# Kernel tuning notes

Hardware: AMD Instinct MI355X
Metric: run time of the kernel (lower is better)

## Reference

```python
import jax, jax.numpy as jnp
import numpy as np

USER_NUM = 100000
ITEM_NUM = 50000
N = USER_NUM + ITEM_NUM
D = 64
NNZ = 2400000
B = 4096
NLEVEL = 3
LEAF = 32
HID = 256
NCLS = 2
NLAYERS = 2
EPS = 0.1
TAU = 0.2


def _l2norm(x, axis=-1):
    return x / jnp.clip(jnp.linalg.norm(x, axis=axis, keepdims=True), 1e-12)


def setup_inputs():
    key = jax.random.key(0)
    ks = jax.random.split(key, 32)
    def w(k, shape):
        fan = shape[-2] if len(shape) >= 2 else shape[-1]
        return jax.random.normal(k, shape, jnp.float32) / np.sqrt(fan)
    z = lambda *s: jnp.zeros(s, jnp.float32)
    return {
        "ego_emb": w(ks[0], (N, D)),
        "gc_w": w(ks[1], (NLAYERS, D, D)), "gc_b": z(NLAYERS, D),
        "bi_w": w(ks[2], (NLAYERS, D, D)), "bi_b": z(NLAYERS, D),
        "uh_w": w(ks[3], (NLEVEL, D, D)), "uh_b": z(NLEVEL, D),
        "ih_w": w(ks[4], (NLEVEL, D, D)), "ih_b": z(NLEVEL, D),
        "ud_w1": w(ks[5], (NLEVEL, D, HID)), "ud_b1": z(NLEVEL, HID),
        "ud_w2": w(ks[6], (NLEVEL, HID, LEAF)), "ud_b2": z(NLEVEL, LEAF),
        "id_w1": w(ks[7], (NLEVEL, D, HID)), "id_b1": z(NLEVEL, HID),
        "id_w2": w(ks[8], (NLEVEL, HID, LEAF)), "id_b2": z(NLEVEL, LEAF),
        "q_w": w(ks[9], (LEAF, LEAF)), "q_b": z(LEAF),
        "k_w": w(ks[10], (LEAF, LEAF)), "k_b": z(LEAF),
        "v_w": w(ks[11], (LEAF, LEAF)), "v_b": z(LEAF),
        "dg_w1": w(ks[12], (NLEVEL * LEAF, D)), "dg_b1": z(D),
        "dg_w2": w(ks[13], (D, D)), "dg_b2": z(D),
        "pr_w": w(ks[14], (D, NCLS)), "pr_b": z(NCLS),
        "adj_vals": jax.random.uniform(ks[15], (NNZ,), jnp.float32) / 16.0,
        "hier_skills": jax.random.uniform(ks[16], (B, NLEVEL * LEAF), jnp.float32),
        "user_id": jax.random.randint(ks[17], (B,), 0, USER_NUM),
        "item_id": jax.random.randint(ks[18], (B,), 0, ITEM_NUM),
        "adj_rows": jax.random.randint(ks[19], (NNZ,), 0, N),
        "adj_cols": jax.random.randint(ks[20], (NNZ,), 0, N),
    }


def _sam(x, q_w, q_b, k_w, k_b, v_w, v_b):
    # x: [B, S, d], single-head self-attention (n_heads=1)
    d = x.shape[-1]
    q = x @ q_w + q_b
    k = x @ k_w + k_b
    v = x @ v_w + v_b
    scores = jnp.einsum('bsd,btd->bst', q, k) / jnp.sqrt(jnp.float32(d))
    attn = jax.nn.softmax(scores, axis=-1)  # softmax over key axis t
    return jnp.einsum('bst,btd->bsd', attn, v)


def _cl_loss(v1, v2):
    n1 = _l2norm(v1)
    n2 = _l2norm(v2)
    pos = jnp.exp(jnp.sum(n1 * n2, -1) / TAU)
    ttl = jnp.sum(jnp.exp(n1 @ n2.T / TAU), axis=1)
    return jnp.mean(-jnp.log(pos / ttl))


def _cl_module(recs, key):
    # recs: [L, B, LEAF]
    noise = jax.random.uniform(key, recs.shape, recs.dtype)
    recs_new = recs + jnp.sign(recs) * _l2norm(noise) * EPS
    return jnp.mean(jax.vmap(_cl_loss)(recs, recs_new))


def reference(ego_emb, gc_w, gc_b, bi_w, bi_b, uh_w, uh_b, ih_w, ih_b,
              ud_w1, ud_b1, ud_w2, ud_b2, id_w1, id_b1, id_w2, id_b2,
              q_w, q_b, k_w, k_b, v_w, v_b, dg_w1, dg_b1, dg_w2, dg_b2,
              pr_w, pr_b, adj_vals, hier_skills, user_id, item_id,
              adj_rows, adj_cols):
    # ---- NGCF propagation: sparse adj matmul + bi-interaction ----
    E = ego_emb
    E_sum = ego_emb
    for l in range(NLAYERS):
        side = jax.ops.segment_sum(adj_vals[:, None] * E[adj_cols], adj_rows,
                                   num_segments=N)  # spmm(adj_norm, E)
        sum_e = jax.nn.leaky_relu(side @ gc_w[l] + gc_b[l])
        bi_e = jax.nn.leaky_relu((E * side) @ bi_w[l] + bi_b[l])
        E = _l2norm(sum_e + bi_e)  # dropout -> identity (eval)
        E_sum = E_sum + E
    ue = E_sum[:USER_NUM][user_id]   # [B, D]
    ie = E_sum[USER_NUM:][item_id]   # [B, D]
    # ---- hierarchy projections + disentangled encoders (stacked over levels) ----
    u_reps = jnp.tanh(jnp.einsum('bd,lde->lbe', ue, uh_w) + uh_b[:, None, :])
    i_reps = jnp.tanh(jnp.einsum('bd,lde->lbe', ie, ih_w) + ih_b[:, None, :])
    u_recs = jnp.einsum('lbh,lhk->lbk',
                        jnp.tanh(jnp.einsum('lbd,ldh->lbh', u_reps, ud_w1) + ud_b1[:, None, :]),
                        ud_w2) + ud_b2[:, None, :]  # [L, B, LEAF]
    i_recs = jnp.einsum('lbh,lhk->lbk',
                        jnp.tanh(jnp.einsum('lbd,ldh->lbh', i_reps, id_w1) + id_b1[:, None, :]),
                        id_w2) + id_b2[:, None, :]
    # ---- self-attention across levels ----
    u_att = _sam(u_recs.transpose(1, 0, 2), q_w, q_b, k_w, k_b, v_w, v_b)  # [B, L, LEAF]
    i_att = _sam(i_recs.transpose(1, 0, 2), q_w, q_b, k_w, k_b, v_w, v_b)
    # ---- contrastive losses (detached in original via torch.Tensor(...)) ----
    kc = jax.random.split(jax.random.key(42), 2)
    cl = _cl_module(u_att.transpose(1, 0, 2), kc[0]) + _cl_module(i_att.transpose(1, 0, 2), kc[1])
    cl = jax.lax.stop_gradient(cl)
    # ---- diagnosis head ----
    skills = hier_skills.reshape(B, NLEVEL, LEAF)
    diag = ((jax.nn.sigmoid(u_att) - jax.nn.sigmoid(i_att)) * skills).reshape(B, NLEVEL * LEAF)
    h = jnp.tanh(diag @ dg_w1 + dg_b1) @ dg_w2 + dg_b2  # dropout -> identity (eval)
    out = jax.nn.softmax(h @ pr_w + pr_b, axis=-1)
    return (out, cl)
```

## Files before the change

kernel.cpp:

```cpp
#include <hip/hip_runtime.h>
#include <stdint.h>
#include <math.h>

#define USER_N 100000
#define NODE_N 150000
#define DD 64
#define NNZE 2400000
#define BB 4096
#define NLV 3
#define LF 32
#define HALF_SZ 196608u
#define NTILE 586
#define NSUB 8
#define SCAP 1024
#define EPB 4096

typedef __attribute__((ext_vector_type(8))) short bf16x8;
typedef __attribute__((ext_vector_type(4))) float f32x4;
typedef __attribute__((ext_vector_type(2))) float f32x2;

#define XCC_ID_IMM 63508

__host__ __device__ inline void tf_block(uint32_t k0, uint32_t k1, uint32_t& x0, uint32_t& x1) {
  uint32_t ks[3] = {k0, k1, k0 ^ k1 ^ 0x1BD11BDAu};
  x0 += ks[0]; x1 += ks[1];
  const int R0[4] = {13, 15, 26, 6};
  const int R1[4] = {17, 29, 16, 24};
#pragma unroll
  for (int i = 0; i < 5; ++i) {
    const int* R = (i & 1) ? R1 : R0;
#pragma unroll
    for (int j = 0; j < 4; ++j) {
      x0 += x1;
      x1 = (x1 << R[j]) | (x1 >> (32 - R[j]));
      x1 ^= x0;
    }
    x0 += ks[(i + 1) % 3];
    x1 += ks[(i + 2) % 3] + (uint32_t)(i + 1);
  }
}

__device__ inline float tf_uniform(uint32_t ka, uint32_t kb, uint32_t m) {
  uint32_t x0, x1;
  bool first = m < HALF_SZ;
  if (first) { x0 = m; x1 = m + HALF_SZ; } else { x0 = m - HALF_SZ; x1 = m; }
  tf_block(ka, kb, x0, x1);
  uint32_t bits = first ? x0 : x1;
  return __uint_as_float((bits >> 9) | 0x3f800000u) - 1.0f;
}

__device__ inline unsigned short f2bf(float x) {
  uint32_t b = __float_as_uint(x);
  return (unsigned short)((b + 0x7FFFu + ((b >> 16) & 1u)) >> 16);
}

__device__ inline unsigned char f2fp8(float x) {
  return (unsigned char)(__builtin_amdgcn_cvt_pk_fp8_f32(x, x, 0, false) & 0xFF);
}

__device__ inline void fp8_fma(float4& acc, uint2 rec, uint32_t wrd) {
  float vv = __uint_as_float(rec.y);
  f32x2 lo = __builtin_amdgcn_cvt_pk_f32_fp8((int)wrd, false);
  f32x2 hi = __builtin_amdgcn_cvt_pk_f32_fp8((int)wrd, true);
  acc.x = fmaf(vv, lo.x, acc.x);
  acc.y = fmaf(vv, lo.y, acc.y);
  acc.z = fmaf(vv, hi.x, acc.z);
  acc.w = fmaf(vv, hi.y, acc.w);
}

__global__ __launch_bounds__(256) void k_init(const float* __restrict__ ego,
                                              uint32_t* __restrict__ E8) {
  int i = blockIdx.x * 256 + threadIdx.x;
  float4 v = ((const float4*)ego)[i];
  int w01 = __builtin_amdgcn_cvt_pk_fp8_f32(v.x, v.y, 0, false);
  int w = __builtin_amdgcn_cvt_pk_fp8_f32(v.z, v.w, w01, true);
  E8[i] = (uint32_t)w;
}

__global__ __launch_bounds__(256) void k_scatter_t(const int* __restrict__ rows,
                                                   const int* __restrict__ cols,
                                                   const float* __restrict__ vals,
                                                   int* __restrict__ cursor,
                                                   uint2* __restrict__ sedge_r) {
  __shared__ int cnt[NTILE];
  __shared__ int curs[NTILE];
  int t = threadIdx.x;
  for (int i = t; i < NTILE; i += 256) cnt[i] = 0;
  __syncthreads();
  int r[16];
  int ebase = blockIdx.x * EPB;
#pragma unroll
  for (int j = 0; j < 16; ++j) {
    int e = ebase + j * 256 + t;
    r[j] = (e < NNZE) ? rows[e] : -1;
    if (r[j] >= 0) atomicAdd(&cnt[r[j] >> 8], 1);
  }
  __syncthreads();
  unsigned myx = __builtin_amdgcn_s_getreg(XCC_ID_IMM) & (NSUB - 1);
  for (int i = t; i < NTILE; i += 256) {
    int c = cnt[i];
    curs[i] = c ? atomicAdd(&cursor[(i * NSUB + (int)myx) * 16], c) : 0;
  }
  __syncthreads();
#pragma unroll
  for (int j = 0; j < 16; ++j) {
    if (r[j] < 0) continue;
    int e = ebase + j * 256 + t;
    int tile = r[j] >> 8;
    uint2 rec = make_uint2((uint32_t)cols[e] | ((uint32_t)(r[j] & 255) << 18),
                           __float_as_uint(vals[e]));
    int p = atomicAdd(&curs[tile], 1);
    if (p < SCAP) {
      sedge_r[(size_t)(tile * NSUB + (int)myx) * SCAP + p] = rec;
    } else {
#pragma unroll 1
      for (int att = 1; att < NSUB; ++att) {
        int seg = tile * NSUB + (int)((myx + att) & (NSUB - 1));
        int p2 = atomicAdd(&cursor[seg * 16], 1);
        if (p2 < SCAP) { sedge_r[(size_t)seg * SCAP + p2] = rec; break; }
      }
    }
  }
}

__global__ __launch_bounds__(1024) void k_scan586(const int* __restrict__ cursor,
                                                  int* __restrict__ out_base,
                                                  int* __restrict__ row_start) {
  __shared__ int buf[1024];
  int t = threadIdx.x;
  int tot = 0;
  if (t < NTILE) {
#pragma unroll
    for (int x = 0; x < NSUB; ++x) {
      int c = cursor[(t * NSUB + x) * 16];
      tot += (c < SCAP) ? c : SCAP;
    }
  }
  buf[t] = tot;
  __syncthreads();
  for (int off = 1; off < 1024; off <<= 1) {
    int add = (t >= off) ? buf[t - off] : 0;
    __syncthreads();
    buf[t] += add;
    __syncthreads();
  }
  if (t < NTILE) out_base[t] = buf[t] - tot;
  if (t == 0) row_start[NODE_N] = NNZE;
}

__global__ __launch_bounds__(256) void k_sort_t(const uint2* __restrict__ sedge_r,
                                                const int* __restrict__ cursor,
                                                const int* __restrict__ out_base,
                                                uint2* __restrict__ sedge,
                                                int* __restrict__ row_start) {
  __shared__ int hist[256], buf[256], curs[256];
  int t = threadIdx.x;
  int tile = blockIdx.x;
  int obase = out_base[tile];
  hist[t] = 0;
  __syncthreads();
#pragma unroll 1
  for (int x = 0; x < NSUB; ++x) {
    int seg = tile * NSUB + x;
    int cnt = cursor[seg * 16];
    if (cnt > SCAP) cnt = SCAP;
    const uint2* sp = sedge_r + (size_t)seg * SCAP;
    for (int i = t; i < cnt; i += 256)
      atomicAdd(&hist[sp[i].x >> 18], 1);
  }
  __syncthreads();
  int v = hist[t];
  buf[t] = v;
  __syncthreads();
  for (int off = 1; off < 256; off <<= 1) {
    int add = (t >= off) ? buf[t - off] : 0;
    __syncthreads();
    buf[t] += add;
    __syncthreads();
  }
  int excl = buf[t] - v;
  curs[t] = excl;
  int row = tile * 256 + t;
  if (row < NODE_N) row_start[row] = obase + excl;
  __syncthreads();
#pragma unroll 1
  for (int x = 0; x < NSUB; ++x) {
    int seg = tile * NSUB + x;
    int cnt = cursor[seg * 16];
    if (cnt > SCAP) cnt = SCAP;
    const uint2* sp = sedge_r + (size_t)seg * SCAP;
    for (int i = t; i < cnt; i += 256) {
      uint2 rec = sp[i];
      int rl = rec.x >> 18;
      int p = atomicAdd(&curs[rl], 1);
      sedge[obase + p] = make_uint2(rec.x & 0x3FFFFu, rec.y);
    }
  }
}

__global__ __launch_bounds__(256) void k_spmm(const uint32_t* __restrict__ E8,
                                              const uint2* __restrict__ sedge,
                                              const int* __restrict__ row_start,
                                              unsigned short* __restrict__ side16,
                                              unsigned short* __restrict__ p16) {
  int r = blockIdx.x * 4 + (threadIdx.x >> 6);
  int lane = threadIdx.x & 63;
  int g = lane >> 4;
  int q = lane & 15;
  int rs = row_start[r], re = row_start[r + 1];
  float4 acc = make_float4(0.f, 0.f, 0.f, 0.f);
  int e = rs;
  for (; e + 16 <= re; e += 16) {
    uint2 e0 = sedge[e + g];
    uint2 e1 = sedge[e + 4 + g];
    uint2 e2 = sedge[e + 8 + g];
    uint2 e3 = sedge[e + 12 + g];
    uint32_t a0 = E8[(size_t)e0.x * 16 + q];
    uint32_t a1 = E8[(size_t)e1.x * 16 + q];
    uint32_t a2 = E8[(size_t)e2.x * 16 + q];
    uint32_t a3 = E8[(size_t)e3.x * 16 + q];
    fp8_fma(acc, e0, a0);
    fp8_fma(acc, e1, a1);
    fp8_fma(acc, e2, a2);
    fp8_fma(acc, e3, a3);
  }
  for (; e + 8 <= re; e += 8) {
    uint2 e0 = sedge[e + g];
    uint2 e1 = sedge[e + 4 + g];
    uint32_t a0 = E8[(size_t)e0.x * 16 + q];
    uint32_t a1 = E8[(size_t)e1.x * 16 + q];
    fp8_fma(acc, e0, a0);
    fp8_fma(acc, e1, a1);
  }
  for (; e + 4 <= re; e += 4) {
    uint2 e0 = sedge[e + g];
    uint32_t a0 = E8[(size_t)e0.x * 16 + q];
    fp8_fma(acc, e0, a0);
  }
  for (; e < re; ++e) {
    if (g == (e & 3)) {
      uint2 e0 = sedge[e];
      uint32_t a0 = E8[(size_t)e0.x * 16 + q];
      fp8_fma(acc, e0, a0);
    }
  }
#pragma unroll
  for (int off = 16; off <= 32; off <<= 1) {
    acc.x += __shfl_xor(acc.x, off, 64);
    acc.y += __shfl_xor(acc.y, off, 64);
    acc.z += __shfl_xor(acc.z, off, 64);
    acc.w += __shfl_xor(acc.w, off, 64);
  }
  if (g == 0) {
    uint32_t ew = E8[(size_t)r * 16 + q];
    f32x2 elo = __builtin_amdgcn_cvt_pk_f32_fp8((int)ew, false);
    f32x2 ehi = __builtin_amdgcn_cvt_pk_f32_fp8((int)ew, true);
    ushort4 s16, pp;
    s16.x = f2bf(acc.x); s16.y = f2bf(acc.y); s16.z = f2bf(acc.z); s16.w = f2bf(acc.w);
    pp.x = f2bf(acc.x * elo.x); pp.y = f2bf(acc.y * elo.y);
    pp.z = f2bf(acc.z * ehi.x); pp.w = f2bf(acc.w * ehi.y);
    *(ushort4*)&side16[(size_t)r * DD + q * 4] = s16;
    *(ushort4*)&p16[(size_t)r * DD + q * 4] = pp;
  }
}

__global__ __launch_bounds__(256) void k_transform(const float* __restrict__ gw,
                                                   const float* __restrict__ gb,
                                                   const float* __restrict__ bw,
                                                   const float* __restrict__ bb,
                                                   const unsigned short* __restrict__ side16,
                                                   const unsigned short* __restrict__ p16,
                                                   float* __restrict__ Eout,
                                                   unsigned char* __restrict__ E8b) {
  int t = threadIdx.x;
  int wv = t >> 6, lane = t & 63;
  int n = lane & 15, quad = lane >> 4;
  bf16x8 wg[4][2], wb[4][2];
  float gbl[4], bbl[4];
#pragma unroll
  for (int c = 0; c < 4; ++c) {
    gbl[c] = gb[c * 16 + n];
    bbl[c] = bb[c * 16 + n];
#pragma unroll
    for (int h = 0; h < 2; ++h) {
#pragma unroll
      for (int j = 0; j < 8; ++j) {
        int k = h * 32 + quad * 8 + j;
        wg[c][h][j] = (short)f2bf(gw[k * 64 + c * 16 + n]);
        wb[c][h][j] = (short)f2bf(bw[k * 64 + c * 16 + n]);
      }
    }
  }
  const f32x4 z = {0.f, 0.f, 0.f, 0.f};
  for (int tile = blockIdx.x * 4 + wv; tile < NODE_N / 16; tile += gridDim.x * 4) {
    int i0 = tile * 16;
    bf16x8 as0 = *(const bf16x8*)&side16[(size_t)(i0 + n) * DD + quad * 8];
    bf16x8 as1 = *(const bf16x8*)&side16[(size_t)(i0 + n) * DD + 32 + quad * 8];
    bf16x8 ap0 = *(const bf16x8*)&p16[(size_t)(i0 + n) * DD + quad * 8];
    bf16x8 ap1 = *(const bf16x8*)&p16[(size_t)(i0 + n) * DD + 32 + quad * 8];
    float v[4][4];
    float sq0 = 0.f, sq1 = 0.f, sq2 = 0.f, sq3 = 0.f;
#pragma unroll
    for (int c = 0; c < 4; ++c) {
      f32x4 ag = __builtin_amdgcn_mfma_f32_16x16x32_bf16(as0, wg[c][0], z, 0, 0, 0);
      ag = __builtin_amdgcn_mfma_f32_16x16x32_bf16(as1, wg[c][1], ag, 0, 0, 0);
      f32x4 ab = __builtin_amdgcn_mfma_f32_16x16x32_bf16(ap0, wb[c][0], z, 0, 0, 0);
      ab = __builtin_amdgcn_mfma_f32_16x16x32_bf16(ap1, wb[c][1], ab, 0, 0, 0);
#pragma unroll
      for (int r = 0; r < 4; ++r) {
        float a1 = ag[r] + gbl[c];
        a1 = (a1 > 0.f) ? a1 : 0.01f * a1;
        float a2 = ab[r] + bbl[c];
        a2 = (a2 > 0.f) ? a2 : 0.01f * a2;
        float vv = a1 + a2;
        v[c][r] = vv;
        if (r == 0) sq0 += vv * vv;
        else if (r == 1) sq1 += vv * vv;
        else if (r == 2) sq2 += vv * vv;
        else sq3 += vv * vv;
      }
    }
#pragma unroll
    for (int off = 1; off < 16; off <<= 1) {
      sq0 += __shfl_xor(sq0, off, 64);
      sq1 += __shfl_xor(sq1, off, 64);
      sq2 += __shfl_xor(sq2, off, 64);
      sq3 += __shfl_xor(sq3, off, 64);
    }
    float inv0 = 1.f / fmaxf(sqrtf(sq0), 1e-12f);
    float inv1 = 1.f / fmaxf(sqrtf(sq1), 1e-12f);
    float inv2 = 1.f / fmaxf(sqrtf(sq2), 1e-12f);
    float inv3 = 1.f / fmaxf(sqrtf(sq3), 1e-12f);
#pragma unroll
    for (int c = 0; c < 4; ++c) {
      float vn0 = v[c][0] * inv0;
      float vn1 = v[c][1] * inv1;
      float vn2 = v[c][2] * inv2;
      float vn3 = v[c][3] * inv3;
      size_t o0 = (size_t)(i0 + quad * 4 + 0) * DD + c * 16 + n;
      size_t o1 = o0 + DD, o2 = o1 + DD, o3 = o2 + DD;
      Eout[o0] = vn0; Eout[o1] = vn1; Eout[o2] = vn2; Eout[o3] = vn3;
      E8b[o0] = f2fp8(vn0); E8b[o1] = f2fp8(vn1);
      E8b[o2] = f2fp8(vn2); E8b[o3] = f2fp8(vn3);
    }
  }
}

__global__ __launch_bounds__(128) void k_gather(const float* __restrict__ ego,
                                                const float* __restrict__ E1,
                                                const float* __restrict__ E2,
                                                const int* __restrict__ uid,
                                                const int* __restrict__ iid,
                                                float* __restrict__ ue, float* __restrict__ ie) {
  int b = blockIdx.x, t = threadIdx.x;
  if (t < 64) {
    size_t o = (size_t)uid[b] * 64 + t;
    ue[(size_t)b * 64 + t] = ego[o] + E1[o] + E2[o];
  } else {
    int d = t - 64;
    size_t o = (size_t)(USER_N + iid[b]) * 64 + d;
    ie[(size_t)b * 64 + d] = ego[o] + E1[o] + E2[o];
  }
}

__global__ __launch_bounds__(256) void k_encoder2(
    const float* __restrict__ ue, const float* __restrict__ ie,
    const float* __restrict__ uh_w, const float* __restrict__ uh_b,
    const float* __restrict__ ud_w1, const float* __restrict__ ud_b1,
    const float* __restrict__ ud_w2, const float* __restrict__ ud_b2,
    const float* __restrict__ ih_w, const float* __restrict__ ih_b,
    const float* __restrict__ id_w1, const float* __restrict__ id_b1,
    const float* __restrict__ id_w2, const float* __restrict__ id_b2,
    float* __restrict__ recs_u, float* __restrict__ recs_i) {
  __shared__ float sx[32][64];
  __shared__ float sr1[32][64];
  __shared__ float st[32][257];
  int t = threadIdx.x;
  int r0 = blockIdx.x * 32;
  int l = blockIdx.y;
  int side = blockIdx.z;
  const float* xin = side ? ie : ue;
  const float* hw = side ? ih_w : uh_w;
  const float* hb = side ? ih_b : uh_b;
  const float* w1 = side ? id_w1 : ud_w1;
  const float* b1 = side ? id_b1 : ud_b1;
  const float* w2 = side ? id_w2 : ud_w2;
  const float* b2 = side ? id_b2 : ud_b2;
  float* recs = side ? recs_i : recs_u;

  {
    const float* src = xin + (size_t)r0 * 64;
#pragma unroll
    for (int j = 0; j < 8; ++j)
      ((float*)sx)[j * 256 + t] = src[j * 256 + t];
  }
  __syncthreads();

  {
    int c = t & 63;
    int rg = (t >> 6) * 8;
    const float* W = hw + (size_t)l * 64 * 64;
    float bias = hb[l * 64 + c];
    float a[8];
#pragma unroll
    for (int j = 0; j < 8; ++j) a[j] = bias;
#pragma unroll 2
    for (int k = 0; k < 64; ++k) {
      float w = W[k * 64 + c];
#pragma unroll
      for (int j = 0; j < 8; ++j) a[j] = fmaf(sx[rg + j][k], w, a[j]);
    }
#pragma unroll
    for (int j = 0; j < 8; ++j) sr1[rg + j][c] = tanhf(a[j]);
  }
  __syncthreads();

  {
    const float* W = w1 + (size_t)l * 64 * 256;
    float bias = b1[l * 256 + t];
    float a[32];
#pragma unroll
    for (int j = 0; j < 32; ++j) a[j] = bias;
#pragma unroll 2
    for (int k = 0; k < 64; ++k) {
      float w = W[k * 256 + t];
#pragma unroll
      for (int j = 0; j < 32; ++j) a[j] = fmaf(sr1[j][k], w, a[j]);
    }
#pragma unroll
    for (int j = 0; j < 32; ++j) st[j][t] = tanhf(a[j]);
  }
  __syncthreads();

  {
    int c = t & 31;
    int rg = (t >> 5) * 4;
    const float* W = w2 + (size_t)l * 256 * 32;
    float bias = b2[l * 32 + c];
    float a[4];
#pragma unroll
    for (int j = 0; j < 4; ++j) a[j] = bias;
#pragma unroll 4
    for (int k = 0; k < 256; ++k) {
      float w = W[k * 32 + c];
#pragma unroll
      for (int j = 0; j < 4; ++j) a[j] = fmaf(st[rg + j][k], w, a[j]);
    }
#pragma unroll
    for (int j = 0; j < 4; ++j)
      recs[((size_t)l * BB + (r0 + rg + j)) * 32 + c] = a[j];
  }
}

__global__ __launch_bounds__(256) void k_attn(const float* __restrict__ recs,
                                              const float* __restrict__ qw, const float* __restrict__ qb,
                                              const float* __restrict__ kw, const float* __restrict__ kb,
                                              const float* __restrict__ vw, const float* __restrict__ vb,
                                              float* __restrict__ att) {
  int t = threadIdx.x;
  int b = blockIdx.x * 8 + (t >> 5);
  int d = t & 31;
  float x0 = recs[((size_t)0 * BB + b) * 32 + d];
  float x1 = recs[((size_t)1 * BB + b) * 32 + d];
  float x2 = recs[((size_t)2 * BB + b) * 32 + d];
  float q0 = qb[d], q1 = q0, q2 = q0;
  float c0 = kb[d], c1 = c0, c2 = c0;
  float v0 = vb[d], v1 = v0, v2 = v0;
#pragma unroll 4
  for (int kk = 0; kk < 32; ++kk) {
    float xa = __shfl(x0, kk, 32);
    float xb = __shfl(x1, kk, 32);
    float xc = __shfl(x2, kk, 32);
    float wq = qw[kk * 32 + d], wk = kw[kk * 32 + d], wv = vw[kk * 32 + d];
    q0 += xa * wq; q1 += xb * wq; q2 += xc * wq;
    c0 += xa * wk; c1 += xb * wk; c2 += xc * wk;
    v0 += xa * wv; v1 += xb * wv; v2 += xc * wv;
  }
  float qs[3] = {q0, q1, q2}, ks[3] = {c0, c1, c2}, vs[3] = {v0, v1, v2};
  float sc[3][3];
#pragma unroll
  for (int s = 0; s < 3; ++s)
#pragma unroll
    for (int u = 0; u < 3; ++u) {
      float p = qs[s] * ks[u];
#pragma unroll
      for (int off = 16; off; off >>= 1) p += __shfl_xor(p, off, 32);
      sc[s][u] = p * 0.17677669529663687f;
    }
#pragma unroll
  for (int s = 0; s < 3; ++s) {
    float m = fmaxf(sc[s][0], fmaxf(sc[s][1], sc[s][2]));
    float e0 = __expf(sc[s][0] - m), e1 = __expf(sc[s][1] - m), e2 = __expf(sc[s][2] - m);
    float inv = 1.f / (e0 + e1 + e2);
    att[(size_t)b * 96 + s * 32 + d] = (e0 * vs[0] + e1 * vs[1] + e2 * vs[2]) * inv;
  }
}

__global__ __launch_bounds__(256) void k_noise(const float* __restrict__ att_u,
                                               const float* __restrict__ att_i,
                                               uint32_t ku0, uint32_t ku1, uint32_t ki0, uint32_t ki1,
                                               unsigned short* __restrict__ n1b,
                                               unsigned short* __restrict__ n2b,
                                               float* __restrict__ posdot) {
  int t = threadIdx.x;
  int g = blockIdx.x * 8 + (t >> 5);
  int k = t & 31;
  int side = g / (NLV * BB);
  int rem = g - side * (NLV * BB);
  int l = rem >> 12;
  int b = rem & 4095;
  const float* att = side ? att_i : att_u;
  uint32_t ka = side ? ki0 : ku0;
  uint32_t kb = side ? ki1 : ku1;
  float r = att[(size_t)b * 96 + l * 32 + k];
  float ss = r * r;
#pragma unroll
  for (int off = 16; off; off >>= 1) ss += __shfl_xor(ss, off, 32);
  float v1 = r / fmaxf(sqrtf(ss), 1e-12f);
  uint32_t m = ((uint32_t)(l * BB + b)) * 32u + (uint32_t)k;
  float u = tf_uniform(ka, kb, m);
  float us = u * u;
#pragma unroll
  for (int off = 16; off; off >>= 1) us += __shfl_xor(us, off, 32);
  float un = u / fmaxf(sqrtf(us), 1e-12f);
  float sgn = (r > 0.f) ? 1.f : ((r < 0.f) ? -1.f : 0.f);
  float rn = r + sgn * un * 0.1f;
  float s2 = rn * rn;
#pragma unroll
  for (int off = 16; off; off >>= 1) s2 += __shfl_xor(s2, off, 32);
  float v2 = rn / fmaxf(sqrtf(s2), 1e-12f);
  float pd = v1 * v2;
#pragma unroll
  for (int off = 16; off; off >>= 1) pd += __shfl_xor(pd, off, 32);
  size_t o = (size_t)g * 32 + k;
  n1b[o] = f2bf(v1);
  n2b[o] = f2bf(v2);
  if (k == 0) posdot[g] = pd;
}

__global__ __launch_bounds__(256) void k_ttl(const unsigned short* __restrict__ n1b,
                                             const unsigned short* __restrict__ n2b,
                                             float* __restrict__ ttl) {
  int t = threadIdx.x;
  int wv = t >> 6, lane = t & 63;
  int sl = blockIdx.x >> 6;
  int istripe = blockIdx.x & 63;
  int i0 = istripe * 64 + wv * 16;
  const unsigned short* ab = n1b + (size_t)sl * BB * 32;
  const unsigned short* bb = n2b + (size_t)sl * BB * 32;
  int m = lane & 15, quad = lane >> 4;
  bf16x8 afrag = *(const bf16x8*)&ab[(size_t)(i0 + m) * 32 + quad * 8];
  float r0a = 0.f, r1a = 0.f, r2a = 0.f, r3a = 0.f;
  f32x4 z = {0.f, 0.f, 0.f, 0.f};
  for (int jt = 0; jt < 256; jt += 4) {
    bf16x8 b0 = *(const bf16x8*)&bb[((size_t)((jt + 0) * 16 + m)) * 32 + quad * 8];
    bf16x8 b1 = *(const bf16x8*)&bb[((size_t)((jt + 1) * 16 + m)) * 32 + quad * 8];
    bf16x8 b2 = *(const bf16x8*)&bb[((size_t)((jt + 2) * 16 + m)) * 32 + quad * 8];
    bf16x8 b3 = *(const bf16x8*)&bb[((size_t)((jt + 3) * 16 + m)) * 32 + quad * 8];
    f32x4 s0 = __builtin_amdgcn_mfma_f32_16x16x32_bf16(afrag, b0, z, 0, 0, 0);
    f32x4 s1 = __builtin_amdgcn_mfma_f32_16x16x32_bf16(afrag, b1, z, 0, 0, 0);
    f32x4 s2 = __builtin_amdgcn_mfma_f32_16x16x32_bf16(afrag, b2, z, 0, 0, 0);
    f32x4 s3 = __builtin_amdgcn_mfma_f32_16x16x32_bf16(afrag, b3, z, 0, 0, 0);
    r0a += __expf(s0.x * 5.f) + __expf(s1.x * 5.f) + __expf(s2.x * 5.f) + __expf(s3.x * 5.f);
    r1a += __expf(s0.y * 5.f) + __expf(s1.y * 5.f) + __expf(s2.y * 5.f) + __expf(s3.y * 5.f);
    r2a += __expf(s0.z * 5.f) + __expf(s1.z * 5.f) + __expf(s2.z * 5.f) + __expf(s3.z * 5.f);
    r3a += __expf(s0.w * 5.f) + __expf(s1.w * 5.f) + __expf(s2.w * 5.f) + __expf(s3.w * 5.f);
  }
#pragma unroll
  for (int off = 1; off < 16; off <<= 1) {
    r0a += __shfl_xor(r0a, off, 64);
    r1a += __shfl_xor(r1a, off, 64);
    r2a += __shfl_xor(r2a, off, 64);
    r3a += __shfl_xor(r3a, off, 64);
  }
  if (m == 0) {
    int rbase = sl * BB + i0 + quad * 4;
    ttl[rbase + 0] = r0a;
    ttl[rbase + 1] = r1a;
    ttl[rbase + 2] = r2a;
    ttl[rbase + 3] = r3a;
  }
}

__global__ __launch_bounds__(1024) void k_clred(const float* __restrict__ ttl,
                                                const float* __restrict__ posdot,
                                                float* __restrict__ outp) {
  __shared__ float red[1024];
  int t = threadIdx.x;
  float a = 0.f;
  for (int idx = t; idx < 6 * BB; idx += 1024)
    a += logf(ttl[idx]) - posdot[idx] * 5.0f;
  red[t] = a;
  __syncthreads();
  for (int off = 512; off; off >>= 1) {
    if (t < off) red[t] += red[t + off];
    __syncthreads();
  }
  if (t == 0) outp[2 * BB] = red[0] * (1.f / 12288.f);
}

__global__ __launch_bounds__(256) void k_head(const float* __restrict__ att_u,
                                              const float* __restrict__ att_i,
                                              const float* __restrict__ skills,
                                              const float* __restrict__ w1, const float* __restrict__ b1,
                                              const float* __restrict__ w2, const float* __restrict__ b2,
                                              const float* __restrict__ pw, const float* __restrict__ pb,
                                              float* __restrict__ outp) {
  __shared__ float diag[4][96], t1[4][64];
  int t = threadIdx.x;
  int w = t >> 6, lane = t & 63;
  int b = blockIdx.x * 4 + w;
  for (int j = lane; j < 96; j += 64) {
    float su = 1.f / (1.f + __expf(-att_u[(size_t)b * 96 + j]));
    float si = 1.f / (1.f + __expf(-att_i[(size_t)b * 96 + j]));
    diag[w][j] = (su - si) * skills[(size_t)b * 96 + j];
  }
  __syncthreads();
  float a = b1[lane];
#pragma unroll 8
  for (int j = 0; j < 96; ++j) a += diag[w][j] * w1[j * 64 + lane];
  t1[w][lane] = tanhf(a);
  __syncthreads();
  float h = b2[lane];
#pragma unroll 8
  for (int kk = 0; kk < 64; ++kk) h += t1[w][kk] * w2[kk * 64 + lane];
  float p0 = h * pw[lane * 2 + 0];
  float p1 = h * pw[lane * 2 + 1];
#pragma unroll
  for (int off = 32; off; off >>= 1) {
    p0 += __shfl_xor(p0, off, 64);
    p1 += __shfl_xor(p1, off, 64);
  }
  if (lane == 0) {
    float l0 = p0 + pb[0], l1 = p1 + pb[1];
    float m = fmaxf(l0, l1);
    float e0 = __expf(l0 - m), e1 = __expf(l1 - m);
    float inv = 1.f / (e0 + e1);
    outp[(size_t)b * 2 + 0] = e0 * inv;
    outp[(size_t)b * 2 + 1] = e1 * inv;
  }
}

extern "C" void kernel_launch(void* const* d_in, const int* in_sizes, int n_in,
                              void* d_out, int out_size, void* d_ws, size_t ws_size,
                              hipStream_t stream) {
  const float* ego    = (const float*)d_in[0];
  const float* gc_w   = (const float*)d_in[1];
  const float* gc_b   = (const float*)d_in[2];
  const float* bi_w   = (const float*)d_in[3];
  const float* bi_b   = (const float*)d_in[4];
  const float* uh_w   = (const float*)d_in[5];
  const float* uh_b   = (const float*)d_in[6];
  const float* ih_w   = (const float*)d_in[7];
  const float* ih_b   = (const float*)d_in[8];
  const float* ud_w1  = (const float*)d_in[9];
  const float* ud_b1  = (const float*)d_in[10];
  const float* ud_w2  = (const float*)d_in[11];
  const float* ud_b2  = (const float*)d_in[12];
  const float* id_w1  = (const float*)d_in[13];
  const float* id_b1  = (const float*)d_in[14];
  const float* id_w2  = (const float*)d_in[15];
  const float* id_b2  = (const float*)d_in[16];
  const float* q_w    = (const float*)d_in[17];
  const float* q_b    = (const float*)d_in[18];
  const float* k_w    = (const float*)d_in[19];
  const float* k_b    = (const float*)d_in[20];
  const float* v_w    = (const float*)d_in[21];
  const float* v_b    = (const float*)d_in[22];
  const float* dg_w1  = (const float*)d_in[23];
  const float* dg_b1  = (const float*)d_in[24];
  const float* dg_w2  = (const float*)d_in[25];
  const float* dg_b2  = (const float*)d_in[26];
  const float* pr_w   = (const float*)d_in[27];
  const float* pr_b   = (const float*)d_in[28];
  const float* adj_vals = (const float*)d_in[29];
  const float* skills = (const float*)d_in[30];
  const int* user_id  = (const int*)d_in[31];
  const int* item_id  = (const int*)d_in[32];
  const int* adj_rows = (const int*)d_in[33];
  const int* adj_cols = (const int*)d_in[34];
  float* outp = (float*)d_out;

  char* w = (char*)d_ws;
  auto alloc = [&](size_t bytes) -> char* {
    char* p = w;
    w += (bytes + 255) & ~(size_t)255;
    return p;
  };
  float* E1     = (float*)alloc((size_t)NODE_N * DD * 4);
  float* E2     = (float*)alloc((size_t)NODE_N * DD * 4);
  uint32_t* E8  = (uint32_t*)alloc((size_t)NODE_N * DD);
  unsigned short* side16 = (unsigned short*)alloc((size_t)NODE_N * DD * 2);
  unsigned short* p16    = (unsigned short*)alloc((size_t)NODE_N * DD * 2);
  uint2* sedge_r= (uint2*)alloc((size_t)NTILE * NSUB * SCAP * 8);
  uint2* sedge  = (uint2*)alloc((size_t)NNZE * 8);
  int*   cursor = (int*)  alloc((size_t)NTILE * NSUB * 16 * 4);
  int*   out_base = (int*)alloc((size_t)(NTILE + 1) * 4);
  int*   row_start = (int*)alloc((size_t)(NODE_N + 1) * 4);
  float* posdot = (float*)alloc((size_t)6 * BB * 4);
  float* ttl    = (float*)alloc((size_t)6 * BB * 4);

  char* ap = (char*)sedge_r;
  auto alias = [&](size_t bytes) -> char* {
    char* p = ap;
    ap += (bytes + 255) & ~(size_t)255;
    return p;
  };
  float* ue     = (float*)alias((size_t)BB * 64 * 4);
  float* ie     = (float*)alias((size_t)BB * 64 * 4);
  float* recs_u = (float*)alias((size_t)NLV * BB * 32 * 4);
  float* recs_i = (float*)alias((size_t)NLV * BB * 32 * 4);
  float* att_u  = (float*)alias((size_t)BB * 96 * 4);
  float* att_i  = (float*)alias((size_t)BB * 96 * 4);
  unsigned short* n1b = (unsigned short*)alias((size_t)6 * BB * 32 * 2);
  unsigned short* n2b = (unsigned short*)alias((size_t)6 * BB * 32 * 2);

  uint32_t a0 = 0, a1 = 2, b0 = 1, b1 = 3;
  tf_block(0u, 42u, a0, a1);
  tf_block(0u, 42u, b0, b1);
  uint32_t ku0 = a0, ku1 = b0;
  uint32_t ki0 = a1, ki1 = b1;

  (void)hipMemsetAsync(cursor, 0, (size_t)NTILE * NSUB * 16 * 4, stream);

  k_init<<<9375, 256, 0, stream>>>(ego, E8);
  k_scatter_t<<<(NNZE + EPB - 1) / EPB, 256, 0, stream>>>(adj_rows, adj_cols, adj_vals,
                                                          cursor, sedge_r);
  k_scan586<<<1, 1024, 0, stream>>>(cursor, out_base, row_start);
  k_sort_t<<<NTILE, 256, 0, stream>>>(sedge_r, cursor, out_base, sedge, row_start);

  float* Ebufs[2] = {E1, E2};
  for (int l = 0; l < 2; ++l) {
    k_spmm<<<37500, 256, 0, stream>>>(E8, sedge, row_start, side16, p16);
    k_transform<<<1172, 256, 0, stream>>>(gc_w + l * 4096, gc_b + l * 64,
                                          bi_w + l * 4096, bi_b + l * 64,
                                          side16, p16, Ebufs[l], (unsigned char*)E8);
  }

  k_gather<<<4096, 128, 0, stream>>>(ego, E1, E2, user_id, item_id, ue, ie);

  dim3 ge(128, 3, 2);
  k_encoder2<<<ge, 256, 0, stream>>>(ue, ie,
                                     uh_w, uh_b, ud_w1, ud_b1, ud_w2, ud_b2,
                                     ih_w, ih_b, id_w1, id_b1, id_w2, id_b2,
                                     recs_u, recs_i);

  k_attn<<<512, 256, 0, stream>>>(recs_u, q_w, q_b, k_w, k_b, v_w, v_b, att_u);
  k_attn<<<512, 256, 0, stream>>>(recs_i, q_w, q_b, k_w, k_b, v_w, v_b, att_i);

  k_noise<<<3072, 256, 0, stream>>>(att_u, att_i, ku0, ku1, ki0, ki1, n1b, n2b, posdot);

  k_ttl<<<384, 256, 0, stream>>>(n1b, n2b, ttl);
  k_clred<<<1, 1024, 0, stream>>>(ttl, posdot, outp);

  k_head<<<1024, 256, 0, stream>>>(att_u, att_i, skills, dg_w1, dg_b1, dg_w2, dg_b2,
                                   pr_w, pr_b, outp);
}
```

Before: 605.2 us.

## Split fp8 embedding into four column slabs and run SpMM per slab

Stores the fp8 embedding table as four column-partitioned slabs of 16 dims each, so each slab is 2.4 MB and may stay resident in cache during gathers. SpMM now runs four passes, one per slab, with 16 edges in flight per wave, packed fp32x2 FMAs and nontemporal edge loads and stores. The transform kernel writes the next layer's fp8 table in the same slab layout. The cost is that the edge list is read four times per layer and the launch count grows.

Result: slower. 926.6 us (+53.1%).

```diff
diff --git a/kernel.cpp b/kernel.cpp
--- a/kernel.cpp
+++ b/kernel.cpp
@@ -58,23 +58,25 @@
   return (unsigned char)(__builtin_amdgcn_cvt_pk_fp8_f32(x, x, 0, false) & 0xFF);
 }
 
-__device__ inline void fp8_fma(float4& acc, uint2 rec, uint32_t wrd) {
-  float vv = __uint_as_float(rec.y);
+__device__ inline void fp8_fma2(f32x2& a01, f32x2& a23, uint32_t vbits, uint32_t wrd) {
+  float vvs = __uint_as_float(vbits);
+  f32x2 vv = {vvs, vvs};
   f32x2 lo = __builtin_amdgcn_cvt_pk_f32_fp8((int)wrd, false);
   f32x2 hi = __builtin_amdgcn_cvt_pk_f32_fp8((int)wrd, true);
-  acc.x = fmaf(vv, lo.x, acc.x);
-  acc.y = fmaf(vv, lo.y, acc.y);
-  acc.z = fmaf(vv, hi.x, acc.z);
-  acc.w = fmaf(vv, hi.y, acc.w);
+  a01 = __builtin_elementwise_fma(vv, lo, a01);
+  a23 = __builtin_elementwise_fma(vv, hi, a23);
 }
 
 __global__ __launch_bounds__(256) void k_init(const float* __restrict__ ego,
-                                              uint32_t* __restrict__ E8) {
+                                              uint32_t* __restrict__ E8q) {
   int i = blockIdx.x * 256 + threadIdx.x;
   float4 v = ((const float4*)ego)[i];
   int w01 = __builtin_amdgcn_cvt_pk_fp8_f32(v.x, v.y, 0, false);
   int w = __builtin_amdgcn_cvt_pk_fp8_f32(v.z, v.w, w01, true);
-  E8[i] = (uint32_t)w;
+  int row = i >> 4;
+  int dq = i & 15;
+  int p = dq >> 2, q = dq & 3;
+  E8q[((size_t)p * NODE_N + row) * 4 + q] = (uint32_t)w;
 }
 
 __global__ __launch_bounds__(256) void k_scatter_t(const int* __restrict__ rows,
@@ -198,69 +200,62 @@
   }
 }
 
-__global__ __launch_bounds__(256) void k_spmm(const uint32_t* __restrict__ E8,
-                                              const uint2* __restrict__ sedge,
-                                              const int* __restrict__ row_start,
-                                              unsigned short* __restrict__ side16,
-                                              unsigned short* __restrict__ p16) {
+__global__ __launch_bounds__(256) void k_spmm4(const uint32_t* __restrict__ E8q,
+                                               const uint2* __restrict__ sedge,
+                                               const int* __restrict__ row_start,
+                                               unsigned short* __restrict__ side16,
+                                               unsigned short* __restrict__ p16,
+                                               int pass) {
   int r = blockIdx.x * 4 + (threadIdx.x >> 6);
   int lane = threadIdx.x & 63;
-  int g = lane >> 4;
-  int q = lane & 15;
+  int g = lane >> 2;
+  int q = lane & 3;
+  const uint32_t* Ep = E8q + (size_t)pass * NODE_N * 4;
   int rs = row_start[r], re = row_start[r + 1];
-  float4 acc = make_float4(0.f, 0.f, 0.f, 0.f);
+  f32x2 a01 = {0.f, 0.f}, a23 = {0.f, 0.f};
   int e = rs;
+  for (; e + 32 <= re; e += 32) {
+    unsigned long long w0 = __builtin_nontemporal_load((const unsigned long long*)&sedge[e + g]);
+    unsigned long long w1 = __builtin_nontemporal_load((const unsigned long long*)&sedge[e + 16 + g]);
+    uint32_t a0 = Ep[(size_t)(uint32_t)w0 * 4 + q];
+    uint32_t a1 = Ep[(size_t)(uint32_t)w1 * 4 + q];
+    fp8_fma2(a01, a23, (uint32_t)(w0 >> 32), a0);
+    fp8_fma2(a01, a23, (uint32_t)(w1 >> 32), a1);
+  }
   for (; e + 16 <= re; e += 16) {
-    uint2 e0 = sedge[e + g];
-    uint2 e1 = sedge[e + 4 + g];
-    uint2 e2 = sedge[e + 8 + g];
-    uint2 e3 = sedge[e + 12 + g];
-    uint32_t a0 = E8[(size_t)e0.x * 16 + q];
-    uint32_t a1 = E8[(size_t)e1.x * 16 + q];
-    uint32_t a2 = E8[(size_t)e2.x * 16 + q];
-    uint32_t a3 = E8[(size_t)e3.x * 16 + q];
-    fp8_fma(acc, e0, a0);
-    fp8_fma(acc, e1, a1);
-    fp8_fma(acc, e2, a2);
-    fp8_fma(acc, e3, a3);
-  }
-  for (; e + 8 <= re; e += 8) {
-    uint2 e0 = sedge[e + g];
-    uint2 e1 = sedge[e + 4 + g];
-    uint32_t a0 = E8[(size_t)e0.x * 16 + q];
-    uint32_t a1 = E8[(size_t)e1.x * 16 + q];
-    fp8_fma(acc, e0, a0);
-    fp8_fma(acc, e1, a1);
-  }
-  for (; e + 4 <= re; e += 4) {
-    uint2 e0 = sedge[e + g];
-    uint32_t a0 = E8[(size_t)e0.x * 16 + q];
-    fp8_fma(acc, e0, a0);
-  }
-  for (; e < re; ++e) {
-    if (g == (e & 3)) {
-      uint2 e0 = sedge[e];
-      uint32_t a0 = E8[(size_t)e0.x * 16 + q];
-      fp8_fma(acc, e0, a0);
-    }
-  }
-#pragma unroll
-  for (int off = 16; off <= 32; off <<= 1) {
-    acc.x += __shfl_xor(acc.x, off, 64);
-    acc.y += __shfl_xor(acc.y, off, 64);
-    acc.z += __shfl_xor(acc.z, off, 64);
-    acc.w += __shfl_xor(acc.w, off, 64);
+    unsigned long long w0 = __builtin_nontemporal_load((const unsigned long long*)&sedge[e + g]);
+    uint32_t a0 = Ep[(size_t)(uint32_t)w0 * 4 + q];
+    fp8_fma2(a01, a23, (uint32_t)(w0 >> 32), a0);
+  }
+  {
+    int ee = e + g;
+    if (ee < re) {
+      unsigned long long w0 = __builtin_nontemporal_load((const unsigned long long*)&sedge[ee]);
+      uint32_t a0 = Ep[(size_t)(uint32_t)w0 * 4 + q];
+      fp8_fma2(a01, a23, (uint32_t)(w0 >> 32), a0);
+    }
+  }
+  float s0 = a01.x, s1 = a01.y, s2 = a23.x, s3 = a23.y;
+#pragma unroll
+  for (int off = 4; off <= 32; off <<= 1) {
+    s0 += __shfl_xor(s0, off, 64);
+    s1 += __shfl_xor(s1, off, 64);
+    s2 += __shfl_xor(s2, off, 64);
+    s3 += __shfl_xor(s3, off, 64);
   }
   if (g == 0) {
-    uint32_t ew = E8[(size_t)r * 16 + q];
+    uint32_t ew = Ep[(size_t)r * 4 + q];
     f32x2 elo = __builtin_amdgcn_cvt_pk_f32_fp8((int)ew, false);
     f32x2 ehi = __builtin_amdgcn_cvt_pk_f32_fp8((int)ew, true);
     ushort4 s16, pp;
-    s16.x = f2bf(acc.x); s16.y = f2bf(acc.y); s16.z = f2bf(acc.z); s16.w = f2bf(acc.w);
-    pp.x = f2bf(acc.x * elo.x); pp.y = f2bf(acc.y * elo.y);
-    pp.z = f2bf(acc.z * ehi.x); pp.w = f2bf(acc.w * ehi.y);
-    *(ushort4*)&side16[(size_t)r * DD + q * 4] = s16;
-    *(ushort4*)&p16[(size_t)r * DD + q * 4] = pp;
+    s16.x = f2bf(s0); s16.y = f2bf(s1); s16.z = f2bf(s2); s16.w = f2bf(s3);
+    pp.x = f2bf(s0 * elo.x); pp.y = f2bf(s1 * elo.y);
+    pp.z = f2bf(s2 * ehi.x); pp.w = f2bf(s3 * ehi.y);
+    size_t o = (size_t)r * DD + pass * 16 + q * 4;
+    __builtin_nontemporal_store(*(unsigned long long*)&s16,
+                                (unsigned long long*)&side16[o]);
+    __builtin_nontemporal_store(*(unsigned long long*)&pp,
+                                (unsigned long long*)&p16[o]);
   }
 }
 
@@ -340,8 +335,11 @@
       size_t o0 = (size_t)(i0 + quad * 4 + 0) * DD + c * 16 + n;
       size_t o1 = o0 + DD, o2 = o1 + DD, o3 = o2 + DD;
       Eout[o0] = vn0; Eout[o1] = vn1; Eout[o2] = vn2; Eout[o3] = vn3;
-      E8b[o0] = f2fp8(vn0); E8b[o1] = f2fp8(vn1);
-      E8b[o2] = f2fp8(vn2); E8b[o3] = f2fp8(vn3);
+      size_t b0 = ((size_t)c * NODE_N + (i0 + quad * 4)) * 16 + n;
+      E8b[b0] = f2fp8(vn0);
+      E8b[b0 + 16] = f2fp8(vn1);
+      E8b[b0 + 32] = f2fp8(vn2);
+      E8b[b0 + 48] = f2fp8(vn3);
     }
   }
 }
@@ -731,7 +729,8 @@
 
   float* Ebufs[2] = {E1, E2};
   for (int l = 0; l < 2; ++l) {
-    k_spmm<<<37500, 256, 0, stream>>>(E8, sedge, row_start, side16, p16);
+    for (int p = 0; p < 4; ++p)
+      k_spmm4<<<37500, 256, 0, stream>>>(E8, sedge, row_start, side16, p16, p);
     k_transform<<<1172, 256, 0, stream>>>(gc_w + l * 4096, gc_b + l * 64,
                                           bi_w + l * 4096, bi_b + l * 64,
                                           side16, p16, Ebufs[l], (unsigned char*)E8);
```
